# Performance work log

Measured on AMD Instinct MI355X. Metric: run time of the kernel, lower is better.

The kernel has to match this reference:

```python
import jax, jax.numpy as jnp
import numpy as np

N = 50000      # nodes
E = 400000     # edges per edge type
T = 4          # edge types: add/sub/mul/div
F_IN = 128     # in_channels
H = 2          # heads
C = 64         # hidden_channels (per head)
HC = H * C     # 128
MLP = C // 8   # hidden_channels // 8 = 8
NUM_CLASSES = 10


def _glorot(key, shape):
    fan_in, fan_out = shape[-2], shape[-1]
    s = jnp.sqrt(6.0 / (fan_in + fan_out))
    return jax.random.uniform(key, shape, jnp.float32, -s, s)


def setup_inputs() -> dict:
    key = jax.random.key(0)
    ks = jax.random.split(key, 12)
    x = jax.random.normal(ks[0], (N, F_IN), jnp.float32)
    edge_index = jax.random.randint(ks[1], (T, 2, E), 0, N, jnp.int32)
    # layer-1 GATv2 params, stacked over the 4 edge types
    Wl1 = _glorot(ks[2], (T, F_IN, HC))
    Wr1 = _glorot(ks[3], (T, F_IN, HC))
    att1 = _glorot(ks[4], (T, H, C))
    b1 = jnp.zeros((T, HC), jnp.float32)
    # layer-2 GATv2 params (input dim = hidden*heads)
    Wl2 = _glorot(ks[5], (T, HC, HC))
    Wr2 = _glorot(ks[6], (T, HC, HC))
    att2 = _glorot(ks[7], (T, H, C))
    b2 = jnp.zeros((T, HC), jnp.float32)
    # MLP head
    W_lin1 = _glorot(ks[8], (HC, MLP))
    b_lin1 = jnp.zeros((MLP,), jnp.float32)
    W_lin2 = _glorot(ks[9], (MLP, NUM_CLASSES))
    b_lin2 = jnp.zeros((NUM_CLASSES,), jnp.float32)
    return dict(x=x, edge_index=edge_index, Wl1=Wl1, Wr1=Wr1, att1=att1, b1=b1,
                Wl2=Wl2, Wr2=Wr2, att2=att2, b2=b2,
                W_lin1=W_lin1, b_lin1=b_lin1, W_lin2=W_lin2, b_lin2=b_lin2)


def gatv2_conv(x, src, dst, Wl, Wr, att, bias):
    """PyG GATv2Conv: add self-loops, per-edge LeakyReLU attention,
    softmax over incoming edges per destination, weighted scatter-add."""
    n = x.shape[0]
    xl = (x @ Wl).reshape(n, H, C)   # source transform
    xr = (x @ Wr).reshape(n, H, C)   # destination transform
    loop = jnp.arange(n, dtype=src.dtype)
    s = jnp.concatenate([src, loop])
    d = jnp.concatenate([dst, loop])
    e = jax.nn.leaky_relu(xl[s] + xr[d], 0.2)          # [E+n, H, C]
    score = jnp.einsum('ehc,hc->eh', e, att)           # [E+n, H]
    smax = jax.ops.segment_max(score, d, num_segments=n)  # [N, H]
    p = jnp.exp(score - smax[d])                       # stable softmax numerators
    denom = jax.ops.segment_sum(p, d, num_segments=n)  # [N, H]
    msg = jax.ops.segment_sum(p[:, :, None] * xl[s], d, num_segments=n)  # [N, H, C]
    out = msg / denom[:, :, None]
    return out.reshape(n, HC) + bias


def hetero_layer(x, edge_index, Wl, Wr, att, b):
    # HeteroConv with aggr='sum' over the 4 edge types (single node type)
    out = gatv2_conv(x, edge_index[0, 0], edge_index[0, 1], Wl[0], Wr[0], att[0], b[0])
    for t in range(1, T):
        out = out + gatv2_conv(x, edge_index[t, 0], edge_index[t, 1], Wl[t], Wr[t], att[t], b[t])
    return out


def reference(x, edge_index, Wl1, Wr1, att1, b1, Wl2, Wr2, att2, b2,
              W_lin1, b_lin1, W_lin2, b_lin2):
    h = jax.nn.relu(hetero_layer(x, edge_index, Wl1, Wr1, att1, b1))
    h = jax.nn.relu(hetero_layer(h, edge_index, Wl2, Wr2, att2, b2))
    h = jax.nn.relu(h @ W_lin1 + b_lin1)
    # dropout p=0.5 is identity at eval time
    return h @ W_lin2 + b_lin2
```

## Files before the change

### kernel.cpp

```cpp
#include <hip/hip_runtime.h>
#include <hip/hip_bf16.h>
#include <math.h>

#define NN 50000
#define EE 400000
#define EEN 450000
#define TT 4
#define FD 128
#define RPS 50004
#define NBKT 196
#define BCAP 4096
#define LOG2E 1.44269504f

typedef __attribute__((ext_vector_type(8))) short bf16x8;
typedef __attribute__((ext_vector_type(4))) float f32x4;

__device__ inline float bf2f(unsigned short u) {
  union { unsigned int i; float f; } x; x.i = ((unsigned int)u) << 16; return x.f;
}
__device__ inline unsigned short f2bf(float f) {
  __hip_bfloat16 h = __float2bfloat16(f);
  unsigned short u; __builtin_memcpy(&u, &h, 2); return u;
}
__device__ inline float blo(unsigned int u) {
  union { unsigned int i; float f; } x; x.i = u << 16; return x.f;
}
__device__ inline float bhi(unsigned int u) {
  union { unsigned int i; float f; } x; x.i = u & 0xFFFF0000u; return x.f;
}
__device__ inline float fexp2(float x) { return __builtin_amdgcn_exp2f(x); }
__device__ inline float sgn04(float a) {
  union { float f; unsigned int i; } x; x.f = a;
  x.i = (x.i & 0x80000000u) | 0x3ECCCCCDu;
  return x.f;
}
__device__ inline float qsum32(float v) {
  v += __builtin_bit_cast(float, __builtin_amdgcn_update_dpp(
         0, __builtin_bit_cast(int, v), 0xB1, 0xF, 0xF, true));
  v += __builtin_bit_cast(float, __builtin_amdgcn_update_dpp(
         0, __builtin_bit_cast(int, v), 0x4E, 0xF, 0xF, true));
  v += __builtin_bit_cast(float, __builtin_amdgcn_update_dpp(
         0, __builtin_bit_cast(int, v), 0x141, 0xF, 0xF, true));
  v += __builtin_bit_cast(float, __builtin_amdgcn_update_dpp(
         0, __builtin_bit_cast(int, v), 0x140, 0xF, 0xF, true));
  v += __builtin_bit_cast(float, __builtin_amdgcn_ds_swizzle(
         __builtin_bit_cast(int, v), 0x401F));
  return v;
}

__global__ void k_cvtW(const float* __restrict__ Wl1, const float* __restrict__ Wr1,
                       const float* __restrict__ Wl2, const float* __restrict__ Wr2,
                       unsigned short* __restrict__ Bpack) {
  const int idx = blockIdx.x * 256 + threadIdx.x;
  const int R = idx >> 14;
  const int kc = idx & 16383;
  const int lr = R & 1, t = (R >> 1) & 3, layer = R >> 3;
  const float* W = layer ? (lr ? Wr2 : Wl2) : (lr ? Wr1 : Wl1);
  const float v = W[t * 16384 + kc];
  const int k = kc >> 7, c = kc & 127;
  const int nt = c >> 4, ks = k >> 5, g = (k >> 3) & 3, j = k & 7;
  const int lane = g * 16 + (c & 15);
  Bpack[(size_t)R * 16384 + ((nt * 4 + ks) * 64 + lane) * 8 + j] = f2bf(v);
}

__global__ void k_cvtA(const float* __restrict__ src, unsigned short* __restrict__ ahi,
                       unsigned short* __restrict__ alo) {
  const int idx = blockIdx.x * 256 + threadIdx.x;
  float4 v = ((const float4*)src)[idx];
  const unsigned short h0 = f2bf(v.x), h1 = f2bf(v.y), h2 = f2bf(v.z), h3 = f2bf(v.w);
  const unsigned short l0 = f2bf(v.x - bf2f(h0)), l1 = f2bf(v.y - bf2f(h1));
  const unsigned short l2 = f2bf(v.z - bf2f(h2)), l3 = f2bf(v.w - bf2f(h3));
  uint2 hv, lv;
  hv.x = (unsigned)h0 | ((unsigned)h1 << 16); hv.y = (unsigned)h2 | ((unsigned)h3 << 16);
  lv.x = (unsigned)l0 | ((unsigned)l1 << 16); lv.y = (unsigned)l2 | ((unsigned)l3 << 16);
  ((uint2*)ahi)[idx] = hv;
  ((uint2*)alo)[idx] = lv;
}

__global__ __launch_bounds__(128) void k_gemm4(
    const unsigned short* __restrict__ Ahi, const unsigned short* __restrict__ Alo,
    const unsigned short* __restrict__ Bbase,
    unsigned short* __restrict__ xl4, unsigned short* __restrict__ xr4) {
  const int t = blockIdx.y;
  const unsigned short* Bpt = Bbase + (size_t)t * 2 * 16384;
  unsigned short* xl = xl4 + (size_t)t * NN * FD;
  unsigned short* xr = xr4 + (size_t)t * NN * FD;
  const int tid = threadIdx.x;
  const int lane = tid & 63;
  const int w = tid >> 6;
  const int rh = lane & 15, g = lane >> 4;
  const int m0 = blockIdx.x * 64 + w * 32;
  f32x4 acc[2][16];
  #pragma unroll
  for (int a = 0; a < 2; ++a)
    #pragma unroll
    for (int b = 0; b < 16; ++b) acc[a][b] = (f32x4){0.f, 0.f, 0.f, 0.f};
  int r0 = m0 + rh;      if (r0 > NN - 1) r0 = NN - 1;
  int r1 = m0 + 16 + rh; if (r1 > NN - 1) r1 = NN - 1;
  #pragma unroll
  for (int ks = 0; ks < 4; ++ks) {
    const int ko = ks * 32 + g * 8;
    const bf16x8 ah0 = *(const bf16x8*)(Ahi + (size_t)r0 * FD + ko);
    const bf16x8 al0 = *(const bf16x8*)(Alo + (size_t)r0 * FD + ko);
    const bf16x8 ah1 = *(const bf16x8*)(Ahi + (size_t)r1 * FD + ko);
    const bf16x8 al1 = *(const bf16x8*)(Alo + (size_t)r1 * FD + ko);
    #pragma unroll
    for (int nt = 0; nt < 16; ++nt) {
      const bf16x8 b = *(const bf16x8*)(Bpt + (nt >> 3) * 16384 +
                                        (((nt & 7) * 4 + ks) * 64 + lane) * 8);
      acc[0][nt] = __builtin_amdgcn_mfma_f32_16x16x32_bf16(ah0, b, acc[0][nt], 0, 0, 0);
      acc[0][nt] = __builtin_amdgcn_mfma_f32_16x16x32_bf16(al0, b, acc[0][nt], 0, 0, 0);
      acc[1][nt] = __builtin_amdgcn_mfma_f32_16x16x32_bf16(ah1, b, acc[1][nt], 0, 0, 0);
      acc[1][nt] = __builtin_amdgcn_mfma_f32_16x16x32_bf16(al1, b, acc[1][nt], 0, 0, 0);
    }
  }
  #pragma unroll
  for (int mt = 0; mt < 2; ++mt)
    #pragma unroll
    for (int nt = 0; nt < 16; ++nt) {
      unsigned short* op = (nt < 8) ? xl : xr;
      const int cb = (nt & 7) * 16 + rh;
      #pragma unroll
      for (int r = 0; r < 4; ++r) {
        const int row = m0 + mt * 16 + g * 4 + r;
        if (row < NN) op[(size_t)row * FD + cb] = f2bf(acc[mt][nt][r]);
      }
    }
}

__global__ __launch_bounds__(256) void k_bucket(const int* __restrict__ ei,
                                                int* __restrict__ bcur,
                                                unsigned int* __restrict__ ebuf) {
  __shared__ int lcnt[NBKT], lbase[NBKT];
  const int t = blockIdx.y, tid = threadIdx.x;
  const int cbase = blockIdx.x * 4096;
  if (tid < NBKT) lcnt[tid] = 0;
  __syncthreads();
  const int* srcp = ei + (size_t)t * 2 * EE;
  const int* dstp = srcp + EE;
  unsigned int pk[16]; int rk[16];
  #pragma unroll
  for (int i = 0; i < 16; ++i) {
    const int e = cbase + i * 256 + tid;
    rk[i] = -1;
    if (e < EEN) {
      int s, dd;
      if (e < EE) { s = srcp[e]; dd = dstp[e]; }
      else        { s = dd = e - EE; }
      const int b = dd >> 8;
      pk[i] = ((unsigned)dd << 16) | (unsigned)s;
      rk[i] = (atomicAdd(&lcnt[b], 1) << 8) | b;
    }
  }
  __syncthreads();
  if (tid < NBKT && lcnt[tid] > 0) lbase[tid] = atomicAdd(&bcur[t * NBKT + tid], lcnt[tid]);
  __syncthreads();
  #pragma unroll
  for (int i = 0; i < 16; ++i) {
    if (rk[i] >= 0) {
      const int b = rk[i] & 255, r = rk[i] >> 8;
      ebuf[((size_t)t * NBKT + b) * BCAP + lbase[b] + r] = pk[i];
    }
  }
}

__global__ void k_bktscan(const int* __restrict__ bcur, int* __restrict__ bbase) {
  __shared__ int s[TT * NBKT];
  const int tid = threadIdx.x;
  int v0 = 0;
  if (tid < TT * NBKT) { v0 = bcur[tid]; s[tid] = v0; }
  __syncthreads();
  #pragma unroll
  for (int off = 1; off < NBKT; off <<= 1) {
    int a = 0;
    if (tid < TT * NBKT && (tid % NBKT) >= off) a = s[tid - off];
    __syncthreads();
    if (tid < TT * NBKT) s[tid] += a;
    __syncthreads();
  }
  if (tid < TT * NBKT) bbase[tid] = s[tid] - v0;
}

__global__ __launch_bounds__(256) void k_scatter3(const unsigned int* __restrict__ ebuf,
                                                  const int* __restrict__ bcur,
                                                  const int* __restrict__ bbase,
                                                  int* __restrict__ rowp,
                                                  int* __restrict__ col) {
  __shared__ int lc[256], sc[256];
  const int b = blockIdx.x, t = blockIdx.y, tid = threadIdx.x;
  const int d0 = b << 8;
  const int nd = (NN - d0 < 256) ? (NN - d0) : 256;
  const int cnt = bcur[t * NBKT + b];
  const int base = bbase[t * NBKT + b];
  const unsigned int* eb = ebuf + ((size_t)t * NBKT + b) * BCAP;
  lc[tid] = 0;
  __syncthreads();
  for (int j = tid; j < cnt; j += 256) {
    atomicAdd(&lc[(eb[j] >> 16) - d0], 1);
  }
  __syncthreads();
  const int v = lc[tid];
  sc[tid] = v;
  __syncthreads();
  #pragma unroll
  for (int off = 1; off < 256; off <<= 1) {
    const int a = (tid >= off) ? sc[tid - off] : 0;
    __syncthreads();
    sc[tid] += a;
    __syncthreads();
  }
  const int excl = base + sc[tid] - v;
  if (tid < nd) rowp[(size_t)t * RPS + d0 + tid] = excl;
  if (b == NBKT - 1 && tid == 0) rowp[(size_t)t * RPS + NN] = EEN;
  lc[tid] = excl;
  __syncthreads();
  for (int j = tid; j < cnt; j += 256) {
    const unsigned int u = eb[j];
    const int pos = atomicAdd(&lc[(u >> 16) - d0], 1);
    col[(size_t)t * EEN + pos] = (int)(u & 0xFFFF);
  }
}

__global__ __launch_bounds__(256) void k_agg7(
    const unsigned short* __restrict__ xl4, const unsigned short* __restrict__ xr4,
    const int* __restrict__ col, const int* __restrict__ rowp,
    const float* __restrict__ att, const float* __restrict__ bias,
    unsigned short* __restrict__ ahi, unsigned short* __restrict__ alo,
    float* __restrict__ hout, const int mode) {
  const int lane = threadIdx.x & 63;
  const int d = blockIdx.x * 4 + (threadIdx.x >> 6);
  const int half = lane >> 5, sub = lane & 31;
  const int byteoff = half * 128 + sub * 4;
  const int choff = half * 64 + sub * 2;
  float o0 = 0.f, o1 = 0.f;
  #pragma unroll
  for (int t = 0; t < TT; ++t) {
    const char* xlt = (const char*)xl4 + (size_t)t * NN * 256;
    const char* xrt = (const char*)xr4 + (size_t)t * NN * 256;
    const int* colt = col + (size_t)t * EEN;
    float2 av = *(const float2*)(att + t * FD + choff);
    av.x *= LOG2E; av.y *= LOG2E;
    const float sa0 = sgn04(av.x), sa1 = sgn04(av.y);
    const unsigned int ur =
        *(const unsigned int*)(xrt + (size_t)d * 256 + byteoff);
    const float axr0 = av.x * blo(ur), axr1 = av.y * bhi(ur);
    float den = 0.f, ac0 = 0.f, ac1 = 0.f;
    const int beg = rowp[t * RPS + d];
    const int end = rowp[t * RPS + d + 1];

    unsigned int xA[4], xB[4];
    auto fetch = [&](int e0, unsigned int* xv) {
      int ci = e0 + (lane & 3);
      ci = (ci < end) ? ci : (end - 1);
      const int cvec = colt[ci];
      #pragma unroll
      for (int j = 0; j < 4; ++j) {
        const int c = __builtin_amdgcn_readlane(cvec, j);
        xv[j] = *(const unsigned int*)(xlt + ((size_t)((unsigned)c << 8)) + byteoff);
      }
    };
    fetch(beg, xA);
    for (int e = beg; e < end; e += 4) {
      if (e + 4 < end) fetch(e + 4, xB);
      #pragma unroll
      for (int j = 0; j < 4; ++j) {
        const float x0 = blo(xA[j]), x1 = bhi(xA[j]);
        const float q0 = fmaf(av.x, x0, axr0), q1 = fmaf(av.y, x1, axr1);
        const float r = fmaf(sa1, fabsf(q1), sa0 * fabsf(q0));
        const float c = qsum32(fmaf(0.6f, q0 + q1, r));
        const float w = (e + j < end) ? fexp2(c) : 0.f;
        den += w;
        ac0 = fmaf(w, x0, ac0);
        ac1 = fmaf(w, x1, ac1);
      }
      #pragma unroll
      for (int j = 0; j < 4; ++j) xA[j] = xB[j];
    }
    const float rden = __builtin_amdgcn_rcpf(den);
    o0 = fmaf(ac0, rden, o0);
    o1 = fmaf(ac1, rden, o1);
  }
  #pragma unroll
  for (int t = 0; t < TT; ++t) {
    const float2 bv = *(const float2*)(bias + t * FD + choff);
    o0 += bv.x; o1 += bv.y;
  }
  if (mode == 0) {
    o0 = fmaxf(o0, 0.f); o1 = fmaxf(o1, 0.f);
    const unsigned short h0 = f2bf(o0), h1 = f2bf(o1);
    const unsigned short l0 = f2bf(o0 - bf2f(h0)), l1 = f2bf(o1 - bf2f(h1));
    *(unsigned int*)((char*)ahi + (size_t)d * 256 + byteoff) =
        (unsigned)h0 | ((unsigned)h1 << 16);
    *(unsigned int*)((char*)alo + (size_t)d * 256 + byteoff) =
        (unsigned)l0 | ((unsigned)l1 << 16);
  } else {
    *(float2*)(hout + (size_t)d * FD + choff) = make_float2(o0, o1);
  }
}

__global__ __launch_bounds__(256) void k_mlp(const float* __restrict__ h,
                                             const float* __restrict__ W1,
                                             const float* __restrict__ b1,
                                             const float* __restrict__ W2,
                                             const float* __restrict__ b2,
                                             float* __restrict__ out) {
  __shared__ float sW1[128 * 8];
  __shared__ float sW2[8 * 10];
  __shared__ float sb1[8], sb2[10];
  for (int i = threadIdx.x; i < 1024; i += 256) sW1[i] = W1[i];
  if (threadIdx.x < 80) sW2[threadIdx.x] = W2[threadIdx.x];
  if (threadIdx.x < 8)  sb1[threadIdx.x] = b1[threadIdx.x];
  if (threadIdx.x < 10) sb2[threadIdx.x] = b2[threadIdx.x];
  __syncthreads();
  const int n = blockIdx.x * 256 + threadIdx.x;
  if (n >= NN) return;
  const float* hn = h + (size_t)n * FD;
  float z[8];
  #pragma unroll
  for (int j = 0; j < 8; ++j) z[j] = sb1[j];
  for (int k = 0; k < FD; k += 4) {
    float4 hv = *(const float4*)(hn + k);
    hv.x = fmaxf(hv.x, 0.f); hv.y = fmaxf(hv.y, 0.f);
    hv.z = fmaxf(hv.z, 0.f); hv.w = fmaxf(hv.w, 0.f);
    #pragma unroll
    for (int j = 0; j < 8; ++j) {
      z[j] += hv.x * sW1[(k + 0) * 8 + j] + hv.y * sW1[(k + 1) * 8 + j]
            + hv.z * sW1[(k + 2) * 8 + j] + hv.w * sW1[(k + 3) * 8 + j];
    }
  }
  #pragma unroll
  for (int j = 0; j < 8; ++j) z[j] = fmaxf(z[j], 0.f);
  float o[10];
  #pragma unroll
  for (int c = 0; c < 10; ++c) o[c] = sb2[c];
  #pragma unroll
  for (int j = 0; j < 8; ++j)
    #pragma unroll
    for (int c = 0; c < 10; ++c) o[c] += z[j] * sW2[j * 10 + c];
  float* op = out + (size_t)n * 10;
  #pragma unroll
  for (int c = 0; c < 10; ++c) op[c] = o[c];
}

extern "C" void kernel_launch(void* const* d_in, const int* in_sizes, int n_in,
                              void* d_out, int out_size, void* d_ws, size_t ws_size,
                              hipStream_t stream) {
  const float* x    = (const float*)d_in[0];
  const int*   ei   = (const int*)d_in[1];
  const float* Wl1  = (const float*)d_in[2];
  const float* Wr1  = (const float*)d_in[3];
  const float* att1 = (const float*)d_in[4];
  const float* b1   = (const float*)d_in[5];
  const float* Wl2  = (const float*)d_in[6];
  const float* Wr2  = (const float*)d_in[7];
  const float* att2 = (const float*)d_in[8];
  const float* b2   = (const float*)d_in[9];
  const float* Wi1  = (const float*)d_in[10];
  const float* bi1  = (const float*)d_in[11];
  const float* Wi2  = (const float*)d_in[12];
  const float* bi2  = (const float*)d_in[13];
  float* out = (float*)d_out;

  char* ws = (char*)d_ws;
  size_t off = 0;
  auto alloc = [&](size_t bytes) {
    void* p = ws + off;
    off = (off + bytes + 255) & ~(size_t)255;
    return p;
  };
  unsigned short* xl4   = (unsigned short*)alloc((size_t)TT * NN * FD * 2);
  unsigned short* xr4   = (unsigned short*)alloc((size_t)TT * NN * FD * 2);
  unsigned short* Ahi   = (unsigned short*)alloc((size_t)NN * FD * 2);
  unsigned short* Alo   = (unsigned short*)alloc((size_t)NN * FD * 2);
  unsigned short* Bpack = (unsigned short*)alloc((size_t)2 * TT * 2 * 16384 * 2);
  int*            col   = (int*)alloc((size_t)TT * EEN * 4);
  int*            rowp  = (int*)alloc((size_t)TT * RPS * 4);
  int*            bcur  = (int*)alloc((size_t)TT * NBKT * 4);
  int*            bbase = (int*)alloc((size_t)TT * NBKT * 4);
  unsigned int*   ebuf  = (unsigned int*)alloc((size_t)TT * NBKT * BCAP * 4);
  float* h2 = (float*)Ahi;

  hipMemsetAsync(bcur, 0, (size_t)TT * NBKT * 4, stream);
  k_cvtW<<<1024, 256, 0, stream>>>(Wl1, Wr1, Wl2, Wr2, Bpack);
  k_bucket<<<dim3(110, TT), 256, 0, stream>>>(ei, bcur, ebuf);
  k_bktscan<<<1, 1024, 0, stream>>>(bcur, bbase);
  k_scatter3<<<dim3(NBKT, TT), 256, 0, stream>>>(ebuf, bcur, bbase, rowp, col);

  k_cvtA<<<6250, 256, 0, stream>>>(x, Ahi, Alo);
  k_gemm4<<<dim3(782, TT), 128, 0, stream>>>(Ahi, Alo, Bpack, xl4, xr4);
  k_agg7<<<12500, 256, 0, stream>>>(xl4, xr4, col, rowp, att1, b1,
                                    Ahi, Alo, nullptr, 0);
  k_gemm4<<<dim3(782, TT), 128, 0, stream>>>(Ahi, Alo, Bpack + (size_t)TT * 2 * 16384,
                                             xl4, xr4);
  k_agg7<<<12500, 256, 0, stream>>>(xl4, xr4, col, rowp, att2, b2,
                                    nullptr, nullptr, h2, 1);
  k_mlp<<<(NN + 255) / 256, 256, 0, stream>>>(h2, Wi1, bi1, Wi2, bi2, out);
}
```

Baseline: 533.2 us.

## Process two edges per wavefront in parallel halves in GATv2 aggregation

The aggregation kernel now splits each 64-lane wavefront into two 32-lane slots. Each slot handles a different edge, and each lane covers 4 channels with 8-byte loads instead of 2 channels with 4-byte loads. The per-head score reduction shrinks from 32 to 16 lanes, dropping the ds_swizzle step, and the loop walks edges two at a time. Partial sums from the two halves are merged with cross-half shuffles. This cuts serial loop iterations and reduction latency per edge, at the cost of wasted lanes when a node has an odd edge count and extra shuffles at the end.

```diff
diff --git a/kernel.cpp b/kernel.cpp
--- a/kernel.cpp
+++ b/kernel.cpp
@@ -34,7 +34,7 @@
   x.i = (x.i & 0x80000000u) | 0x3ECCCCCDu;
   return x.f;
 }
-__device__ inline float qsum32(float v) {
+__device__ inline float qsum16(float v) {
   v += __builtin_bit_cast(float, __builtin_amdgcn_update_dpp(
          0, __builtin_bit_cast(int, v), 0xB1, 0xF, 0xF, true));
   v += __builtin_bit_cast(float, __builtin_amdgcn_update_dpp(
@@ -43,8 +43,6 @@
          0, __builtin_bit_cast(int, v), 0x141, 0xF, 0xF, true));
   v += __builtin_bit_cast(float, __builtin_amdgcn_update_dpp(
          0, __builtin_bit_cast(int, v), 0x140, 0xF, 0xF, true));
-  v += __builtin_bit_cast(float, __builtin_amdgcn_ds_swizzle(
-         __builtin_bit_cast(int, v), 0x401F));
   return v;
 }
 
@@ -221,7 +219,7 @@
   }
 }
 
-__global__ __launch_bounds__(256) void k_agg7(
+__global__ __launch_bounds__(256) void k_agg8(
     const unsigned short* __restrict__ xl4, const unsigned short* __restrict__ xr4,
     const int* __restrict__ col, const int* __restrict__ rowp,
     const float* __restrict__ att, const float* __restrict__ bias,
@@ -229,72 +227,82 @@
     float* __restrict__ hout, const int mode) {
   const int lane = threadIdx.x & 63;
   const int d = blockIdx.x * 4 + (threadIdx.x >> 6);
-  const int half = lane >> 5, sub = lane & 31;
-  const int byteoff = half * 128 + sub * 4;
-  const int choff = half * 64 + sub * 2;
-  float o0 = 0.f, o1 = 0.f;
+  const int slot = lane >> 5;
+  const int head = (lane >> 4) & 1, sub = lane & 15;
+  const int byteoff = head * 128 + sub * 8;
+  const int choff = head * 64 + sub * 4;
+  float o0 = 0.f, o1 = 0.f, o2 = 0.f, o3 = 0.f;
   #pragma unroll
   for (int t = 0; t < TT; ++t) {
     const char* xlt = (const char*)xl4 + (size_t)t * NN * 256;
     const char* xrt = (const char*)xr4 + (size_t)t * NN * 256;
     const int* colt = col + (size_t)t * EEN;
-    float2 av = *(const float2*)(att + t * FD + choff);
-    av.x *= LOG2E; av.y *= LOG2E;
+    float4 av = *(const float4*)(att + t * FD + choff);
+    av.x *= LOG2E; av.y *= LOG2E; av.z *= LOG2E; av.w *= LOG2E;
     const float sa0 = sgn04(av.x), sa1 = sgn04(av.y);
-    const unsigned int ur =
-        *(const unsigned int*)(xrt + (size_t)d * 256 + byteoff);
-    const float axr0 = av.x * blo(ur), axr1 = av.y * bhi(ur);
-    float den = 0.f, ac0 = 0.f, ac1 = 0.f;
+    const float sa2 = sgn04(av.z), sa3 = sgn04(av.w);
+    const uint2 ur = *(const uint2*)(xrt + (size_t)d * 256 + byteoff);
+    const float axr0 = av.x * blo(ur.x), axr1 = av.y * bhi(ur.x);
+    const float axr2 = av.z * blo(ur.y), axr3 = av.w * bhi(ur.y);
+    float den = 0.f, a0 = 0.f, a1 = 0.f, a2 = 0.f, a3 = 0.f;
     const int beg = rowp[t * RPS + d];
     const int end = rowp[t * RPS + d + 1];
 
-    unsigned int xA[4], xB[4];
-    auto fetch = [&](int e0, unsigned int* xv) {
-      int ci = e0 + (lane & 3);
+    uint2 xA, xB;
+    auto fetch = [&](int e0) -> uint2 {
+      int ci = e0 + slot;
       ci = (ci < end) ? ci : (end - 1);
-      const int cvec = colt[ci];
-      #pragma unroll
-      for (int j = 0; j < 4; ++j) {
-        const int c = __builtin_amdgcn_readlane(cvec, j);
-        xv[j] = *(const unsigned int*)(xlt + ((size_t)((unsigned)c << 8)) + byteoff);
-      }
+      const unsigned int c = (unsigned)colt[ci];
+      return *(const uint2*)(xlt + ((size_t)c << 8) + byteoff);
     };
-    fetch(beg, xA);
-    for (int e = beg; e < end; e += 4) {
-      if (e + 4 < end) fetch(e + 4, xB);
-      #pragma unroll
-      for (int j = 0; j < 4; ++j) {
-        const float x0 = blo(xA[j]), x1 = bhi(xA[j]);
-        const float q0 = fmaf(av.x, x0, axr0), q1 = fmaf(av.y, x1, axr1);
-        const float r = fmaf(sa1, fabsf(q1), sa0 * fabsf(q0));
-        const float c = qsum32(fmaf(0.6f, q0 + q1, r));
-        const float w = (e + j < end) ? fexp2(c) : 0.f;
-        den += w;
-        ac0 = fmaf(w, x0, ac0);
-        ac1 = fmaf(w, x1, ac1);
-      }
-      #pragma unroll
-      for (int j = 0; j < 4; ++j) xA[j] = xB[j];
-    }
+    xA = fetch(beg);
+    for (int e = beg; e < end; e += 2) {
+      if (e + 2 < end) xB = fetch(e + 2);
+      const float x0 = blo(xA.x), x1 = bhi(xA.x);
+      const float x2 = blo(xA.y), x3 = bhi(xA.y);
+      const float q0 = fmaf(av.x, x0, axr0), q1 = fmaf(av.y, x1, axr1);
+      const float q2 = fmaf(av.z, x2, axr2), q3 = fmaf(av.w, x3, axr3);
+      float r = sa0 * fabsf(q0);
+      r = fmaf(sa1, fabsf(q1), r);
+      r = fmaf(sa2, fabsf(q2), r);
+      r = fmaf(sa3, fabsf(q3), r);
+      const float c = qsum16(fmaf(0.6f, (q0 + q1) + (q2 + q3), r));
+      const float w = (e + slot < end) ? fexp2(c) : 0.f;
+      den += w;
+      a0 = fmaf(w, x0, a0); a1 = fmaf(w, x1, a1);
+      a2 = fmaf(w, x2, a2); a3 = fmaf(w, x3, a3);
+      xA = xB;
+    }
+    den += __shfl_xor(den, 32);
     const float rden = __builtin_amdgcn_rcpf(den);
-    o0 = fmaf(ac0, rden, o0);
-    o1 = fmaf(ac1, rden, o1);
-  }
+    o0 = fmaf(a0, rden, o0); o1 = fmaf(a1, rden, o1);
+    o2 = fmaf(a2, rden, o2); o3 = fmaf(a3, rden, o3);
+  }
+  o0 += __shfl_xor(o0, 32); o1 += __shfl_xor(o1, 32);
+  o2 += __shfl_xor(o2, 32); o3 += __shfl_xor(o3, 32);
   #pragma unroll
   for (int t = 0; t < TT; ++t) {
-    const float2 bv = *(const float2*)(bias + t * FD + choff);
-    o0 += bv.x; o1 += bv.y;
-  }
-  if (mode == 0) {
-    o0 = fmaxf(o0, 0.f); o1 = fmaxf(o1, 0.f);
-    const unsigned short h0 = f2bf(o0), h1 = f2bf(o1);
-    const unsigned short l0 = f2bf(o0 - bf2f(h0)), l1 = f2bf(o1 - bf2f(h1));
-    *(unsigned int*)((char*)ahi + (size_t)d * 256 + byteoff) =
-        (unsigned)h0 | ((unsigned)h1 << 16);
-    *(unsigned int*)((char*)alo + (size_t)d * 256 + byteoff) =
-        (unsigned)l0 | ((unsigned)l1 << 16);
-  } else {
-    *(float2*)(hout + (size_t)d * FD + choff) = make_float2(o0, o1);
+    const float4 bv = *(const float4*)(bias + t * FD + choff);
+    o0 += bv.x; o1 += bv.y; o2 += bv.z; o3 += bv.w;
+  }
+  if (lane < 32) {
+    if (mode == 0) {
+      o0 = fmaxf(o0, 0.f); o1 = fmaxf(o1, 0.f);
+      o2 = fmaxf(o2, 0.f); o3 = fmaxf(o3, 0.f);
+      const unsigned short h0 = f2bf(o0), h1 = f2bf(o1);
+      const unsigned short h2 = f2bf(o2), h3 = f2bf(o3);
+      const unsigned short l0 = f2bf(o0 - bf2f(h0)), l1 = f2bf(o1 - bf2f(h1));
+      const unsigned short l2 = f2bf(o2 - bf2f(h2)), l3 = f2bf(o3 - bf2f(h3));
+      uint2 hv, lv;
+      hv.x = (unsigned)h0 | ((unsigned)h1 << 16);
+      hv.y = (unsigned)h2 | ((unsigned)h3 << 16);
+      lv.x = (unsigned)l0 | ((unsigned)l1 << 16);
+      lv.y = (unsigned)l2 | ((unsigned)l3 << 16);
+      *(uint2*)((char*)ahi + (size_t)d * 256 + byteoff) = hv;
+      *(uint2*)((char*)alo + (size_t)d * 256 + byteoff) = lv;
+    } else {
+      *(float4*)(hout + (size_t)d * FD + choff) = make_float4(o0, o1, o2, o3);
+    }
   }
 }
 
@@ -388,11 +396,11 @@
 
   k_cvtA<<<6250, 256, 0, stream>>>(x, Ahi, Alo);
   k_gemm4<<<dim3(782, TT), 128, 0, stream>>>(Ahi, Alo, Bpack, xl4, xr4);
-  k_agg7<<<12500, 256, 0, stream>>>(xl4, xr4, col, rowp, att1, b1,
+  k_agg8<<<12500, 256, 0, stream>>>(xl4, xr4, col, rowp, att1, b1,
                                     Ahi, Alo, nullptr, 0);
   k_gemm4<<<dim3(782, TT), 128, 0, stream>>>(Ahi, Alo, Bpack + (size_t)TT * 2 * 16384,
                                              xl4, xr4);
-  k_agg7<<<12500, 256, 0, stream>>>(xl4, xr4, col, rowp, att2, b2,
+  k_agg8<<<12500, 256, 0, stream>>>(xl4, xr4, col, rowp, att2, b2,
                                     nullptr, nullptr, h2, 1);
   k_mlp<<<(NN + 255) / 256, 256, 0, stream>>>(h2, Wi1, bi1, Wi2, bi2, out);
 }
```

Measured after the change: 565.1 us. 6.0% more time.
